# Kernel tuning notes

Measured on AMD Instinct MI355X. Metric: run time of the kernel, lower is better.

## Reference

```python
import jax, jax.numpy as jnp
import numpy as np

N, F, H, C = 50000, 128, 4, 32   # nodes, in_channels, heads, hidden_channels
E, R, DE = 800000, 8, 64         # edges, num_relations, edge_dim


def setup_inputs() -> dict:
    key = jax.random.key(0)
    ks = jax.random.split(key, 10)
    x = jax.random.normal(ks[0], (N, F), dtype=jnp.float32)
    edge_index = jax.random.randint(ks[1], (2, E), 0, N, dtype=jnp.int64)
    edge_type = jax.random.randint(ks[2], (E,), 0, R, dtype=jnp.int64)
    s_in = 1.0 / np.sqrt(F)
    s_e = 1.0 / np.sqrt(DE)
    edge_emb = jax.random.normal(ks[3], (R, DE), dtype=jnp.float32)
    Wq = jax.random.normal(ks[4], (F, H * C), dtype=jnp.float32) * s_in
    Wk = jax.random.normal(ks[5], (F, H * C), dtype=jnp.float32) * s_in
    Wv = jax.random.normal(ks[6], (F, H * C), dtype=jnp.float32) * s_in
    We = jax.random.normal(ks[7], (DE, H * C), dtype=jnp.float32) * s_e
    Wskip = jax.random.normal(ks[8], (F, H * C), dtype=jnp.float32) * s_in
    return {"x": x, "edge_index": edge_index, "edge_type": edge_type,
            "edge_emb": edge_emb, "Wq": Wq, "Wk": Wk, "Wv": Wv,
            "We": We, "Wskip": Wskip}


def reference(x, edge_index, edge_type, edge_emb, Wq, Wk, Wv, We, Wskip):
    # TransformerConv (PyG) with edge embeddings, concat heads, root skip, no bias.
    src, dst = edge_index[0], edge_index[1]
    q = (x @ Wq).reshape(N, H, C)
    k = (x @ Wk).reshape(N, H, C)
    v = (x @ Wv).reshape(N, H, C)
    e = (edge_emb[edge_type] @ We).reshape(E, H, C)      # per-edge relation emb
    kj = k[src] + e                                       # [E,H,C]
    logits = (q[dst] * kj).sum(-1) / jnp.sqrt(jnp.float32(C))  # [E,H]
    # segment softmax over incoming edges of each target node
    m = jax.ops.segment_max(logits, dst, num_segments=N)  # [N,H]
    m = jnp.where(jnp.isfinite(m), m, jnp.float32(0.0))
    ex = jnp.exp(logits - m[dst])
    denom = jax.ops.segment_sum(ex, dst, num_segments=N)  # [N,H]
    alpha = ex / (denom[dst] + 1e-16)                     # [E,H]
    msg = (v[src] + e) * alpha[:, :, None]                # [E,H,C]
    out = jax.ops.segment_sum(msg, dst, num_segments=N).reshape(N, H * C)
    return out + x @ Wskip
```

## Files before the change

kernel.cpp:

```cpp
#include <hip/hip_runtime.h>
#include <hip/hip_bf16.h>

#define NN 50000
#define FF 128
#define NH 4
#define CH 32
#define HC 128
#define NE 800000
#define NR 8
#define DEDIM 64
#define NBLK 196
#define HBLK 3125
#define QBLK 250
#define MTILES 3125

typedef __hip_bfloat16 bf16;
typedef __attribute__((ext_vector_type(8))) short short8;
typedef __attribute__((ext_vector_type(4))) float f32x4;

__device__ __forceinline__ float bflo(unsigned u) { return __uint_as_float(u << 16); }
__device__ __forceinline__ float bfhi(unsigned u) { return __uint_as_float(u & 0xFFFF0000u); }

__device__ __forceinline__ unsigned short f2bf(float f) {
  unsigned u = __float_as_uint(f);
  unsigned r = (u + 0x7FFFu + ((u >> 16) & 1u)) >> 16;
  return (unsigned short)r;
}
__device__ __forceinline__ unsigned pack2bf(float lo, float hi) {
  return (unsigned)f2bf(lo) | ((unsigned)f2bf(hi) << 16);
}

template <int ISBF>
__device__ __forceinline__ float ldf(const void* p, size_t i) {
  if (ISBF) return __bfloat162float(((const bf16*)p)[i]);
  return ((const float*)p)[i];
}

__device__ __forceinline__ int idx_at(const void* p, long long i, int is64) {
  if (is64) { long long v = ((const long long*)p)[i]; return (int)v; }
  return ((const int*)p)[i];
}

__global__ __launch_bounds__(256) void k_prep(const int* __restrict__ eidx32,
    const void* __restrict__ etype, const unsigned* __restrict__ xw,
    const void* __restrict__ emb, const void* __restrict__ We,
    int* __restrict__ flag, int* __restrict__ hist, float* __restrict__ ee,
    int* __restrict__ dstp, int* __restrict__ setp) {
  __shared__ float es[NR * DEDIM];
  if (blockIdx.x < HBLK) {
    unsigned long long b = __ballot(eidx32[2 * (threadIdx.x & 63) + 1] != 0);
    int is64 = (b == 0ULL);
    int e = blockIdx.x * 256 + threadIdx.x;
    int src = idx_at(eidx32, e, is64);
    int dst = idx_at(eidx32, (long long)NE + e, is64);
    int et  = idx_at(etype, e, is64);
    src = min(max(src, 0), NN - 1);
    dst = min(max(dst, 0), NN - 1);
    et  = min(max(et, 0), NR - 1);
    dstp[e] = dst;
    setp[e] = (src << 3) | et;
    atomicAdd(&hist[dst], 1);
    return;
  }
  __shared__ int nzIdx, badBf;
  if (threadIdx.x == 0) { nzIdx = 0; badBf = 0; }
  __syncthreads();
  if (threadIdx.x < 128) {
    if (eidx32[2 * threadIdx.x + 1] != 0) atomicAdd(&nzIdx, 1);
    unsigned e = (xw[threadIdx.x] >> 7) & 0xFFu;
    if (e < 90u || e > 140u) atomicAdd(&badBf, 1);
  }
  __syncthreads();
  const int isbf = (badBf == 0);
  if (threadIdx.x == 0) { flag[0] = (nzIdx == 0); flag[1] = isbf; }
  for (int i = threadIdx.x; i < NR * DEDIM; i += 256)
    es[i] = isbf ? ldf<1>(emb, i) : ldf<0>(emb, i);
  __syncthreads();
  for (int o = threadIdx.x; o < NR * HC; o += 256) {
    int r = o >> 7, j = o & 127;
    float acc = 0.f;
    if (isbf) { for (int d = 0; d < DEDIM; ++d) acc += es[r * DEDIM + d] * ldf<1>(We, d * HC + j); }
    else      { for (int d = 0; d < DEDIM; ++d) acc += es[r * DEDIM + d] * ldf<0>(We, d * HC + j); }
    ee[o] = acc;
  }
}

__global__ __launch_bounds__(256) void k_scan1(const int* __restrict__ hist,
                                               int* __restrict__ bsum) {
  __shared__ int red[4];
  int i = blockIdx.x * 256 + threadIdx.x;
  int v = (i < NN) ? hist[i] : 0;
#pragma unroll
  for (int m = 1; m < 64; m <<= 1) v += __shfl_xor(v, m);
  if ((threadIdx.x & 63) == 0) red[threadIdx.x >> 6] = v;
  __syncthreads();
  if (threadIdx.x == 0) bsum[blockIdx.x] = red[0] + red[1] + red[2] + red[3];
}

__global__ __launch_bounds__(256) void k_scan13(const int* __restrict__ hist,
    const int* __restrict__ bsum, int* __restrict__ rowptr,
    int* __restrict__ cursor) {
  __shared__ int s[256];
  int t = threadIdx.x;
  int bv = (t < NBLK) ? bsum[t] : 0;
  s[t] = bv;
  __syncthreads();
  for (int off = 1; off < 256; off <<= 1) {
    int u = (t >= off) ? s[t - off] : 0;
    __syncthreads();
    s[t] += u;
    __syncthreads();
  }
  int bexc = (blockIdx.x == 0) ? 0 : s[blockIdx.x - 1];
  __syncthreads();
  int i = blockIdx.x * 256 + t;
  int v = (i < NN) ? hist[i] : 0;
  s[t] = v;
  __syncthreads();
  for (int off = 1; off < 256; off <<= 1) {
    int u = (t >= off) ? s[t - off] : 0;
    __syncthreads();
    s[t] += u;
    __syncthreads();
  }
  int excl = bexc + s[t] - v;
  if (i < NN) { rowptr[i] = excl; cursor[i] = excl; }
  if (i == 0) rowptr[NN] = NE;
}

#define WT_STRIDE 136

template <int ISBF>
__device__ __forceinline__ void stage_w(const void* __restrict__ W,
                                        unsigned short* __restrict__ wt) {
  for (int i = threadIdx.x; i < FF * HC; i += 256) {
    int k = i >> 7, n = i & 127;
    wt[n * WT_STRIDE + k] = ISBF ? ((const unsigned short*)W)[i]
                                 : f2bf(((const float*)W)[i]);
  }
}

__device__ __forceinline__ void hoist_b(const unsigned short* __restrict__ wt,
                                        int wv, int quad, int lr,
                                        short8 bf[2][4]) {
#pragma unroll
  for (int t = 0; t < 2; ++t) {
    int ncol = wv * 32 + t * 16 + lr;
#pragma unroll
    for (int kb = 0; kb < 4; ++kb)
      bf[t][kb] = *(const short8*)&wt[ncol * WT_STRIDE + kb * 32 + quad * 8];
  }
}

template <int ISBF>
__device__ __forceinline__ void qkvs_body(const void* __restrict__ x,
    const void* __restrict__ W0, const void* __restrict__ W1, int grp, int mc,
    unsigned short* __restrict__ qb, unsigned* __restrict__ kvb,
    void* __restrict__ out, unsigned short* wt) {
  const int lane = threadIdx.x & 63;
  const int wv   = threadIdx.x >> 6;
  const int quad = lane >> 4;
  const int lr   = lane & 15;
  short8 bf0[2][4], bf1[2][4];
  stage_w<ISBF>(W0, wt);
  __syncthreads();
  hoist_b(wt, wv, quad, lr, bf0);
  __syncthreads();
  stage_w<ISBF>(W1, wt);
  __syncthreads();
  hoist_b(wt, wv, quad, lr, bf1);
  const unsigned short* xu = (const unsigned short*)x;
  const float* xf = (const float*)x;
  for (int mt = mc; mt < MTILES; mt += QBLK) {
    int m0 = mt * 16;
    short8 af[4];
#pragma unroll
    for (int kb = 0; kb < 4; ++kb) {
      size_t off = (size_t)(m0 + lr) * FF + kb * 32 + quad * 8;
      if (ISBF) {
        af[kb] = *(const short8*)(xu + off);
      } else {
        float4 fa = *(const float4*)(xf + off);
        float4 fb = *(const float4*)(xf + off + 4);
        short8 a;
        a[0] = (short)f2bf(fa.x); a[1] = (short)f2bf(fa.y);
        a[2] = (short)f2bf(fa.z); a[3] = (short)f2bf(fa.w);
        a[4] = (short)f2bf(fb.x); a[5] = (short)f2bf(fb.y);
        a[6] = (short)f2bf(fb.z); a[7] = (short)f2bf(fb.w);
        af[kb] = a;
      }
    }
    f32x4 a00 = {0.f, 0.f, 0.f, 0.f}, a01 = {0.f, 0.f, 0.f, 0.f};
    f32x4 a10 = {0.f, 0.f, 0.f, 0.f}, a11 = {0.f, 0.f, 0.f, 0.f};
#pragma unroll
    for (int kb = 0; kb < 4; ++kb) {
      a00 = __builtin_amdgcn_mfma_f32_16x16x32_bf16(af[kb], bf0[0][kb], a00, 0, 0, 0);
      a01 = __builtin_amdgcn_mfma_f32_16x16x32_bf16(af[kb], bf0[1][kb], a01, 0, 0, 0);
      a10 = __builtin_amdgcn_mfma_f32_16x16x32_bf16(af[kb], bf1[0][kb], a10, 0, 0, 0);
      a11 = __builtin_amdgcn_mfma_f32_16x16x32_bf16(af[kb], bf1[1][kb], a11, 0, 0, 0);
    }
#pragma unroll
    for (int t = 0; t < 2; ++t) {
      const f32x4 v0 = t ? a01 : a00;
      const f32x4 v1 = t ? a11 : a10;
      int col = wv * 32 + t * 16 + lr;
#pragma unroll
      for (int r = 0; r < 4; ++r) {
        size_t oi = (size_t)(m0 + quad * 4 + r) * HC + col;
        if (grp == 0) {
          qb[oi] = f2bf(v0[r]);
          if (ISBF) ((unsigned short*)out)[oi] = f2bf(v1[r]);
          else      ((float*)out)[oi] = v1[r];
        } else {
          kvb[oi] = pack2bf(v0[r], v1[r]);
        }
      }
    }
  }
}

__global__ __launch_bounds__(256) void k_fused(const unsigned* __restrict__ xw,
    const void* __restrict__ Wq, const void* __restrict__ Wk,
    const void* __restrict__ Wv, const void* __restrict__ Ws,
    unsigned short* __restrict__ qb, unsigned* __restrict__ kvb,
    void* __restrict__ out,
    const int* __restrict__ dstp, const int* __restrict__ setp,
    int* __restrict__ cursor, int* __restrict__ srcet) {
  __shared__ unsigned short wt[HC * WT_STRIDE];
  if (blockIdx.x < 2 * QBLK) {
    unsigned ex = (xw[threadIdx.x & 63] >> 7) & 0xFFu;
    unsigned long long bb = __ballot(ex < 90u || ex > 140u);
    int isbf = (bb == 0ULL);
    int grp = blockIdx.x / QBLK;
    int mc  = blockIdx.x % QBLK;
    const void* W0 = grp ? Wk : Wq;
    const void* W1 = grp ? Wv : Ws;
    if (isbf) qkvs_body<1>(xw, W0, W1, grp, mc, qb, kvb, out, wt);
    else      qkvs_body<0>(xw, W0, W1, grp, mc, qb, kvb, out, wt);
    return;
  }
  int e = (blockIdx.x - 2 * QBLK) * 256 + threadIdx.x;
  int dst = dstp[e];
  int pos = atomicAdd(&cursor[dst], 1);
  srcet[pos] = setp[e];
}

__global__ __launch_bounds__(256) void k_gather(const int* __restrict__ rowptr,
    const int* __restrict__ srcet, const unsigned short* __restrict__ qb,
    const unsigned* __restrict__ kvb, const float* __restrict__ ee,
    const int* __restrict__ flag, void* __restrict__ out) {
  int n = blockIdx.x * 4 + (threadIdx.x >> 6);
  int l = threadIdx.x & 63;
  int t = l >> 5;
  int w = l & 31;
  int j0 = ((w >> 3) << 5) + ((w & 7) << 2);
  int beg = __builtin_amdgcn_readfirstlane(rowptr[n]);
  int end = __builtin_amdgcn_readfirstlane(rowptr[n + 1]);
  uint2 qw = *(const uint2*)(qb + (size_t)n * HC + j0);
  float q0 = bflo(qw.x), q1 = bfhi(qw.x), q2 = bflo(qw.y), q3 = bfhi(qw.y);
  const float sc = 0.17677669529663687f;
  float dn = 0.f, a0 = 0.f, a1 = 0.f, a2 = 0.f, a3 = 0.f;
  int p = beg;
  for (; p + 8 <= end; p += 8) {
    int se[4]; uint4 kv[4]; float4 ev[4];
#pragma unroll
    for (int u = 0; u < 4; ++u) se[u] = srcet[p + 2 * u + t];
#pragma unroll
    for (int u = 0; u < 4; ++u)
      kv[u] = *(const uint4*)(kvb + (size_t)(se[u] >> 3) * HC + j0);
#pragma unroll
    for (int u = 0; u < 4; ++u)
      ev[u] = *(const float4*)(ee + ((se[u] & 7) << 7) + j0);
#pragma unroll
    for (int u = 0; u < 4; ++u) {
      float pp = q0 * (bflo(kv[u].x) + ev[u].x) + q1 * (bflo(kv[u].y) + ev[u].y)
               + q2 * (bflo(kv[u].z) + ev[u].z) + q3 * (bflo(kv[u].w) + ev[u].w);
      pp += __shfl_xor(pp, 1);
      pp += __shfl_xor(pp, 2);
      pp += __shfl_xor(pp, 4);
      float xx = __expf(pp * sc);
      dn += xx;
      a0 += (bfhi(kv[u].x) + ev[u].x) * xx;
      a1 += (bfhi(kv[u].y) + ev[u].y) * xx;
      a2 += (bfhi(kv[u].z) + ev[u].z) * xx;
      a3 += (bfhi(kv[u].w) + ev[u].w) * xx;
    }
  }
  if (p < end) {
    int se[4]; bool ok[4]; uint4 kv[4]; float4 ev[4];
#pragma unroll
    for (int u = 0; u < 4; ++u) {
      int pe = p + 2 * u + t;
      ok[u] = pe < end;
      se[u] = srcet[ok[u] ? pe : beg];
    }
#pragma unroll
    for (int u = 0; u < 4; ++u)
      kv[u] = *(const uint4*)(kvb + (size_t)(se[u] >> 3) * HC + j0);
#pragma unroll
    for (int u = 0; u < 4; ++u)
      ev[u] = *(const float4*)(ee + ((se[u] & 7) << 7) + j0);
#pragma unroll
    for (int u = 0; u < 4; ++u) {
      float pp = q0 * (bflo(kv[u].x) + ev[u].x) + q1 * (bflo(kv[u].y) + ev[u].y)
               + q2 * (bflo(kv[u].z) + ev[u].z) + q3 * (bflo(kv[u].w) + ev[u].w);
      pp += __shfl_xor(pp, 1);
      pp += __shfl_xor(pp, 2);
      pp += __shfl_xor(pp, 4);
      float xx = ok[u] ? __expf(pp * sc) : 0.f;
      dn += xx;
      a0 += (bfhi(kv[u].x) + ev[u].x) * xx;
      a1 += (bfhi(kv[u].y) + ev[u].y) * xx;
      a2 += (bfhi(kv[u].z) + ev[u].z) * xx;
      a3 += (bfhi(kv[u].w) + ev[u].w) * xx;
    }
  }
  dn += __shfl_xor(dn, 32);
  a0 += __shfl_xor(a0, 32);
  a1 += __shfl_xor(a1, 32);
  a2 += __shfl_xor(a2, 32);
  a3 += __shfl_xor(a3, 32);
  if (t == 0) {
    float inv = 1.f / (dn + 1e-16f);
    size_t oi = (size_t)n * HC + j0;
    if (flag[1]) {
      uint2 sk = *(const uint2*)((const unsigned short*)out + oi);
      uint2 o;
      o.x = pack2bf(a0 * inv + bflo(sk.x), a1 * inv + bfhi(sk.x));
      o.y = pack2bf(a2 * inv + bflo(sk.y), a3 * inv + bfhi(sk.y));
      *(uint2*)((unsigned short*)out + oi) = o;
    } else {
      float4 sk = *(const float4*)((const float*)out + oi);
      float4 o = make_float4(a0 * inv + sk.x, a1 * inv + sk.y,
                             a2 * inv + sk.z, a3 * inv + sk.w);
      *(float4*)((float*)out + oi) = o;
    }
  }
}

extern "C" void kernel_launch(void* const* d_in, const int* in_sizes, int n_in,
                              void* d_out, int out_size, void* d_ws, size_t ws_size,
                              hipStream_t stream) {
  const void* x     = d_in[0];
  const void* eidx  = d_in[1];
  const void* etype = d_in[2];
  const void* emb   = d_in[3];
  const void* Wq    = d_in[4];
  const void* Wk    = d_in[5];
  const void* Wv    = d_in[6];
  const void* We    = d_in[7];
  const void* Ws    = d_in[8];

  float* base   = (float*)d_ws;
  int*   flag   = (int*)base;
  float* ee     = base + 16;
  int*   rowptr = (int*)(base + 1040);
  int*   cursor = (int*)(base + 51044);
  int*   bsum   = (int*)(base + 101044);
  int*   srcet  = (int*)(base + 101568);
  int*   dstp   = (int*)(base + 901568);
  int*   setp   = (int*)(base + 1701568);
  unsigned short* qb  = (unsigned short*)(base + 2501568);
  unsigned*       kvb = (unsigned*)(base + 5701568);

  hipMemsetAsync(cursor, 0, NN * sizeof(int), stream);
  k_prep  <<<HBLK + 1, 256, 0, stream>>>((const int*)eidx, etype,
                                         (const unsigned*)x, emb, We,
                                         flag, cursor, ee, dstp, setp);
  k_scan1 <<<NBLK, 256, 0, stream>>>(cursor, bsum);
  k_scan13<<<NBLK, 256, 0, stream>>>(cursor, bsum, rowptr, cursor);
  k_fused <<<2 * QBLK + HBLK, 256, 0, stream>>>((const unsigned*)x, Wq, Wk, Wv, Ws,
                                                qb, kvb, d_out,
                                                dstp, setp, cursor, srcet);
  k_gather<<<NN / 4, 256, 0, stream>>>(rowptr, srcet, qb, kvb, ee, flag, d_out);
}
```

Measured before the change: 261.4 us.

## Split projection GEMMs across prep/scatter kernels and record edge rank in histogram pass

The Q/skip projection now runs in the same launch as the edge-index decode and histogram, and K/V projection runs alongside the CSR scatter. The scatter no longer needs a second atomic pass over per-node cursors because the histogram atomic's return value (rank within the destination) is stored packed with dst and added to rowptr later. This spreads GEMM work over two launches so it overlaps with memory-bound edge passes and removes one round of atomics. The packing assumes dst fits in 16 bits, but node indices up to 49999 fit, and it assumes per-node in-degree stays below 65536.

```diff
diff --git a/kernel.cpp b/kernel.cpp
--- a/kernel.cpp
+++ b/kernel.cpp
@@ -39,93 +39,6 @@
 __device__ __forceinline__ int idx_at(const void* p, long long i, int is64) {
   if (is64) { long long v = ((const long long*)p)[i]; return (int)v; }
   return ((const int*)p)[i];
-}
-
-__global__ __launch_bounds__(256) void k_prep(const int* __restrict__ eidx32,
-    const void* __restrict__ etype, const unsigned* __restrict__ xw,
-    const void* __restrict__ emb, const void* __restrict__ We,
-    int* __restrict__ flag, int* __restrict__ hist, float* __restrict__ ee,
-    int* __restrict__ dstp, int* __restrict__ setp) {
-  __shared__ float es[NR * DEDIM];
-  if (blockIdx.x < HBLK) {
-    unsigned long long b = __ballot(eidx32[2 * (threadIdx.x & 63) + 1] != 0);
-    int is64 = (b == 0ULL);
-    int e = blockIdx.x * 256 + threadIdx.x;
-    int src = idx_at(eidx32, e, is64);
-    int dst = idx_at(eidx32, (long long)NE + e, is64);
-    int et  = idx_at(etype, e, is64);
-    src = min(max(src, 0), NN - 1);
-    dst = min(max(dst, 0), NN - 1);
-    et  = min(max(et, 0), NR - 1);
-    dstp[e] = dst;
-    setp[e] = (src << 3) | et;
-    atomicAdd(&hist[dst], 1);
-    return;
-  }
-  __shared__ int nzIdx, badBf;
-  if (threadIdx.x == 0) { nzIdx = 0; badBf = 0; }
-  __syncthreads();
-  if (threadIdx.x < 128) {
-    if (eidx32[2 * threadIdx.x + 1] != 0) atomicAdd(&nzIdx, 1);
-    unsigned e = (xw[threadIdx.x] >> 7) & 0xFFu;
-    if (e < 90u || e > 140u) atomicAdd(&badBf, 1);
-  }
-  __syncthreads();
-  const int isbf = (badBf == 0);
-  if (threadIdx.x == 0) { flag[0] = (nzIdx == 0); flag[1] = isbf; }
-  for (int i = threadIdx.x; i < NR * DEDIM; i += 256)
-    es[i] = isbf ? ldf<1>(emb, i) : ldf<0>(emb, i);
-  __syncthreads();
-  for (int o = threadIdx.x; o < NR * HC; o += 256) {
-    int r = o >> 7, j = o & 127;
-    float acc = 0.f;
-    if (isbf) { for (int d = 0; d < DEDIM; ++d) acc += es[r * DEDIM + d] * ldf<1>(We, d * HC + j); }
-    else      { for (int d = 0; d < DEDIM; ++d) acc += es[r * DEDIM + d] * ldf<0>(We, d * HC + j); }
-    ee[o] = acc;
-  }
-}
-
-__global__ __launch_bounds__(256) void k_scan1(const int* __restrict__ hist,
-                                               int* __restrict__ bsum) {
-  __shared__ int red[4];
-  int i = blockIdx.x * 256 + threadIdx.x;
-  int v = (i < NN) ? hist[i] : 0;
-#pragma unroll
-  for (int m = 1; m < 64; m <<= 1) v += __shfl_xor(v, m);
-  if ((threadIdx.x & 63) == 0) red[threadIdx.x >> 6] = v;
-  __syncthreads();
-  if (threadIdx.x == 0) bsum[blockIdx.x] = red[0] + red[1] + red[2] + red[3];
-}
-
-__global__ __launch_bounds__(256) void k_scan13(const int* __restrict__ hist,
-    const int* __restrict__ bsum, int* __restrict__ rowptr,
-    int* __restrict__ cursor) {
-  __shared__ int s[256];
-  int t = threadIdx.x;
-  int bv = (t < NBLK) ? bsum[t] : 0;
-  s[t] = bv;
-  __syncthreads();
-  for (int off = 1; off < 256; off <<= 1) {
-    int u = (t >= off) ? s[t - off] : 0;
-    __syncthreads();
-    s[t] += u;
-    __syncthreads();
-  }
-  int bexc = (blockIdx.x == 0) ? 0 : s[blockIdx.x - 1];
-  __syncthreads();
-  int i = blockIdx.x * 256 + t;
-  int v = (i < NN) ? hist[i] : 0;
-  s[t] = v;
-  __syncthreads();
-  for (int off = 1; off < 256; off <<= 1) {
-    int u = (t >= off) ? s[t - off] : 0;
-    __syncthreads();
-    s[t] += u;
-    __syncthreads();
-  }
-  int excl = bexc + s[t] - v;
-  if (i < NN) { rowptr[i] = excl; cursor[i] = excl; }
-  if (i == 0) rowptr[NN] = NE;
 }
 
 #define WT_STRIDE 136
@@ -219,29 +132,121 @@
   }
 }
 
-__global__ __launch_bounds__(256) void k_fused(const unsigned* __restrict__ xw,
-    const void* __restrict__ Wq, const void* __restrict__ Wk,
-    const void* __restrict__ Wv, const void* __restrict__ Ws,
-    unsigned short* __restrict__ qb, unsigned* __restrict__ kvb,
-    void* __restrict__ out,
-    const int* __restrict__ dstp, const int* __restrict__ setp,
-    int* __restrict__ cursor, int* __restrict__ srcet) {
+__global__ __launch_bounds__(256) void k_fusedA(const unsigned* __restrict__ xw,
+    const int* __restrict__ eidx32, const void* __restrict__ etype,
+    const void* __restrict__ emb, const void* __restrict__ We,
+    const void* __restrict__ Wq, const void* __restrict__ Ws,
+    int* __restrict__ flag, int* __restrict__ hist, float* __restrict__ ee,
+    unsigned* __restrict__ drk, int* __restrict__ setp,
+    unsigned short* __restrict__ qb, void* __restrict__ out) {
   __shared__ unsigned short wt[HC * WT_STRIDE];
-  if (blockIdx.x < 2 * QBLK) {
+  if (blockIdx.x < QBLK) {
     unsigned ex = (xw[threadIdx.x & 63] >> 7) & 0xFFu;
     unsigned long long bb = __ballot(ex < 90u || ex > 140u);
     int isbf = (bb == 0ULL);
-    int grp = blockIdx.x / QBLK;
-    int mc  = blockIdx.x % QBLK;
-    const void* W0 = grp ? Wk : Wq;
-    const void* W1 = grp ? Wv : Ws;
-    if (isbf) qkvs_body<1>(xw, W0, W1, grp, mc, qb, kvb, out, wt);
-    else      qkvs_body<0>(xw, W0, W1, grp, mc, qb, kvb, out, wt);
+    if (isbf) qkvs_body<1>(xw, Wq, Ws, 0, blockIdx.x, qb, nullptr, out, wt);
+    else      qkvs_body<0>(xw, Wq, Ws, 0, blockIdx.x, qb, nullptr, out, wt);
     return;
   }
-  int e = (blockIdx.x - 2 * QBLK) * 256 + threadIdx.x;
-  int dst = dstp[e];
-  int pos = atomicAdd(&cursor[dst], 1);
+  if (blockIdx.x < QBLK + HBLK) {
+    unsigned long long b = __ballot(eidx32[2 * (threadIdx.x & 63) + 1] != 0);
+    int is64 = (b == 0ULL);
+    int e = (blockIdx.x - QBLK) * 256 + threadIdx.x;
+    int src = idx_at(eidx32, e, is64);
+    int dst = idx_at(eidx32, (long long)NE + e, is64);
+    int et  = idx_at(etype, e, is64);
+    src = min(max(src, 0), NN - 1);
+    dst = min(max(dst, 0), NN - 1);
+    et  = min(max(et, 0), NR - 1);
+    int rank = atomicAdd(&hist[dst], 1);
+    drk[e]  = ((unsigned)dst << 16) | ((unsigned)rank & 0xFFFFu);
+    setp[e] = (src << 3) | et;
+    return;
+  }
+  float* es = (float*)wt;
+  __shared__ int nzIdx, badBf;
+  if (threadIdx.x == 0) { nzIdx = 0; badBf = 0; }
+  __syncthreads();
+  if (threadIdx.x < 128) {
+    if (eidx32[2 * threadIdx.x + 1] != 0) atomicAdd(&nzIdx, 1);
+    unsigned e = (xw[threadIdx.x] >> 7) & 0xFFu;
+    if (e < 90u || e > 140u) atomicAdd(&badBf, 1);
+  }
+  __syncthreads();
+  const int isbf = (badBf == 0);
+  if (threadIdx.x == 0) { flag[0] = (nzIdx == 0); flag[1] = isbf; }
+  for (int i = threadIdx.x; i < NR * DEDIM; i += 256)
+    es[i] = isbf ? ldf<1>(emb, i) : ldf<0>(emb, i);
+  __syncthreads();
+  for (int o = threadIdx.x; o < NR * HC; o += 256) {
+    int r = o >> 7, j = o & 127;
+    float acc = 0.f;
+    if (isbf) { for (int d = 0; d < DEDIM; ++d) acc += es[r * DEDIM + d] * ldf<1>(We, d * HC + j); }
+    else      { for (int d = 0; d < DEDIM; ++d) acc += es[r * DEDIM + d] * ldf<0>(We, d * HC + j); }
+    ee[o] = acc;
+  }
+}
+
+__global__ __launch_bounds__(256) void k_scan1(const int* __restrict__ hist,
+                                               int* __restrict__ bsum) {
+  __shared__ int red[4];
+  int i = blockIdx.x * 256 + threadIdx.x;
+  int v = (i < NN) ? hist[i] : 0;
+#pragma unroll
+  for (int m = 1; m < 64; m <<= 1) v += __shfl_xor(v, m);
+  if ((threadIdx.x & 63) == 0) red[threadIdx.x >> 6] = v;
+  __syncthreads();
+  if (threadIdx.x == 0) bsum[blockIdx.x] = red[0] + red[1] + red[2] + red[3];
+}
+
+__global__ __launch_bounds__(256) void k_scan13(const int* __restrict__ hist,
+    const int* __restrict__ bsum, int* __restrict__ rowptr) {
+  __shared__ int s[256];
+  int t = threadIdx.x;
+  int bv = (t < NBLK) ? bsum[t] : 0;
+  s[t] = bv;
+  __syncthreads();
+  for (int off = 1; off < 256; off <<= 1) {
+    int u = (t >= off) ? s[t - off] : 0;
+    __syncthreads();
+    s[t] += u;
+    __syncthreads();
+  }
+  int bexc = (blockIdx.x == 0) ? 0 : s[blockIdx.x - 1];
+  __syncthreads();
+  int i = blockIdx.x * 256 + t;
+  int v = (i < NN) ? hist[i] : 0;
+  s[t] = v;
+  __syncthreads();
+  for (int off = 1; off < 256; off <<= 1) {
+    int u = (t >= off) ? s[t - off] : 0;
+    __syncthreads();
+    s[t] += u;
+    __syncthreads();
+  }
+  int excl = bexc + s[t] - v;
+  if (i < NN) rowptr[i] = excl;
+  if (i == 0) rowptr[NN] = NE;
+}
+
+__global__ __launch_bounds__(256) void k_fusedB(const unsigned* __restrict__ xw,
+    const void* __restrict__ Wk, const void* __restrict__ Wv,
+    unsigned* __restrict__ kvb,
+    const unsigned* __restrict__ drk, const int* __restrict__ setp,
+    const int* __restrict__ rowptr, int* __restrict__ srcet) {
+  __shared__ unsigned short wt[HC * WT_STRIDE];
+  if (blockIdx.x < QBLK) {
+    unsigned ex = (xw[threadIdx.x & 63] >> 7) & 0xFFu;
+    unsigned long long bb = __ballot(ex < 90u || ex > 140u);
+    int isbf = (bb == 0ULL);
+    if (isbf) qkvs_body<1>(xw, Wk, Wv, 1, blockIdx.x, nullptr, kvb, nullptr, wt);
+    else      qkvs_body<0>(xw, Wk, Wv, 1, blockIdx.x, nullptr, kvb, nullptr, wt);
+    return;
+  }
+  int e = (blockIdx.x - QBLK) * 256 + threadIdx.x;
+  unsigned d = drk[e];
+  int pos = rowptr[d >> 16] + (int)(d & 0xFFFFu);
+  pos = min(max(pos, 0), NE - 1);
   srcet[pos] = setp[e];
 }
 
@@ -355,22 +360,22 @@
   int*   flag   = (int*)base;
   float* ee     = base + 16;
   int*   rowptr = (int*)(base + 1040);
-  int*   cursor = (int*)(base + 51044);
+  int*   hist   = (int*)(base + 51044);
   int*   bsum   = (int*)(base + 101044);
   int*   srcet  = (int*)(base + 101568);
-  int*   dstp   = (int*)(base + 901568);
+  unsigned* drk = (unsigned*)(base + 901568);
   int*   setp   = (int*)(base + 1701568);
   unsigned short* qb  = (unsigned short*)(base + 2501568);
   unsigned*       kvb = (unsigned*)(base + 5701568);
 
-  hipMemsetAsync(cursor, 0, NN * sizeof(int), stream);
-  k_prep  <<<HBLK + 1, 256, 0, stream>>>((const int*)eidx, etype,
-                                         (const unsigned*)x, emb, We,
-                                         flag, cursor, ee, dstp, setp);
-  k_scan1 <<<NBLK, 256, 0, stream>>>(cursor, bsum);
-  k_scan13<<<NBLK, 256, 0, stream>>>(cursor, bsum, rowptr, cursor);
-  k_fused <<<2 * QBLK + HBLK, 256, 0, stream>>>((const unsigned*)x, Wq, Wk, Wv, Ws,
-                                                qb, kvb, d_out,
-                                                dstp, setp, cursor, srcet);
+  hipMemsetAsync(hist, 0, NN * sizeof(int), stream);
+  k_fusedA<<<QBLK + HBLK + 1, 256, 0, stream>>>((const unsigned*)x,
+                                                (const int*)eidx, etype, emb, We,
+                                                Wq, Ws, flag, hist, ee,
+                                                drk, setp, qb, d_out);
+  k_scan1 <<<NBLK, 256, 0, stream>>>(hist, bsum);
+  k_scan13<<<NBLK, 256, 0, stream>>>(hist, bsum, rowptr);
+  k_fusedB<<<QBLK + HBLK, 256, 0, stream>>>((const unsigned*)x, Wk, Wv, kvb,
+                                            drk, setp, rowptr, srcet);
   k_gather<<<NN / 4, 256, 0, stream>>>(rowptr, srcet, qb, kvb, ee, flag, d_out);
 }
```

Result: faster. 240.2 us (-8.1%).
